# Kernel optimization log

Measured on AMD Instinct MI355X. Metric: run time of the kernel, lower is better.

## Reference

```python
import jax, jax.numpy as jnp
import numpy as np

EDGE_WIDTH = 128
NUM_HEADS = 8
DOT_DIM = EDGE_WIDTH // NUM_HEADS  # 16
B, N = 2, 256


def _layernorm(x, g, b, eps=1e-5):
    mu = jnp.mean(x, axis=-1, keepdims=True)
    var = jnp.var(x, axis=-1, keepdims=True)
    return (x - mu) * jax.lax.rsqrt(var + eps) * g + b


def setup_inputs() -> dict:
    key = jax.random.key(0)
    ks = jax.random.split(key, 8)
    W = EDGE_WIDTH
    H = NUM_HEADS
    s = lambda fan_in: 1.0 / np.sqrt(fan_in)
    return {
        "e": jax.random.normal(ks[0], (B, N, N, W), dtype=jnp.float32),
        "mask": jnp.zeros((B, N, N, 1), dtype=jnp.float32),
        "ln_g": jnp.ones((W,), dtype=jnp.float32),
        "ln_b": jnp.zeros((W,), dtype=jnp.float32),
        "W_V": jax.random.uniform(ks[1], (W, 2 * W), jnp.float32, -s(W), s(W)),
        "b_V": jnp.zeros((2 * W,), dtype=jnp.float32),
        "W_E": jax.random.uniform(ks[2], (W, 2 * H), jnp.float32, -s(W), s(W)),
        "b_E": jnp.zeros((2 * H,), dtype=jnp.float32),
        "W_O": jax.random.uniform(ks[3], (2 * W, W), jnp.float32, -s(2 * W), s(2 * W)),
        "b_O": jnp.zeros((W,), dtype=jnp.float32),
    }


def reference(e, mask, ln_g, ln_b, W_V, b_V, W_E, b_E, W_O, b_O):
    bsize, num_edges, _, embed_dim = e.shape
    H, D = NUM_HEADS, DOT_DIM

    e_ln = _layernorm(e, ln_g, ln_b)

    V = e_ln @ W_V + b_V                       # [B,N,N,2W]
    V_in, V_out = jnp.split(V, 2, axis=-1)     # each [B,N,N,W]
    V_in = V_in.reshape(bsize, num_edges, num_edges, D, H)
    V_out = V_out.reshape(bsize, num_edges, num_edges, D, H)

    E = e_ln @ W_E + b_E                       # [B,N,N,2H]
    E_in, E_out = jnp.split(E, 2, axis=-1)     # each [B,N,N,H]

    # NOTE: original module computes a scale factor but never applies it.
    A_in = jax.nn.softmax(E_in + mask, axis=2)            # softmax over k
    Va_in = jnp.einsum('bikh,bjkdh->bijdh', A_in, V_in)

    A_out = jax.nn.softmax(E_out + mask, axis=1)          # softmax over k
    Va_out = jnp.einsum('bkih,bkjdh->bijdh', A_out, V_out)

    Va = jnp.concatenate([Va_in, Va_out], axis=-1)        # [B,N,N,D,2H]
    Va = Va.reshape(bsize, num_edges, num_edges, embed_dim * 2)
    return Va @ W_O + b_O
```

## Files before the change

### kernel.cpp

```cpp
#include <hip/hip_runtime.h>
#include <hip/hip_bf16.h>
#include <stdint.h>


typedef short short8 __attribute__((ext_vector_type(8)));
typedef short short4v __attribute__((ext_vector_type(4)));
typedef float floatx4 __attribute__((ext_vector_type(4)));

#define AS1(p) ((const __attribute__((address_space(1))) void*)(p))
#define AS3(p) ((__attribute__((address_space(3))) void*)(p))

__device__ inline short f2bf(float v) {
    uint32_t u = __builtin_bit_cast(uint32_t, v);
    u += 0x7FFFu + ((u >> 16) & 1u);
    return (short)(u >> 16);
}

__global__ __launch_bounds__(128) void k0_prep(const float* __restrict__ WV,
                                               const float* __restrict__ WE,
                                               const float* __restrict__ WO,
                                               short* __restrict__ Wcat2,
                                               short* __restrict__ WOt2,
                                               const float* __restrict__ bV,
                                               const float* __restrict__ bE,
                                               float* __restrict__ bcat) {
    int bx = blockIdx.x, t = threadIdx.x;
    if (bx < 288) {
        int v = bx / 144, n = bx % 144, k = t;
        float val = 0.f;
        if (n < 128) val = WV[k * 256 + v * 128 + n];
        else if (n < 136) val = WE[k * 16 + v * 8 + (n - 128)];
        Wcat2[(v * 144 + n) * 128 + k] = f2bf(val);
    } else if (bx < 320) {
        int cc = bx - 288;
        for (int j = 0; j < 8; ++j) {
            int c = cc * 8 + j;
            WOt2[(cc * 128 + t) * 8 + j] =
                f2bf(WO[((c & 15) * 16 + (c >> 4)) * 128 + t]);
        }
    } else {
        for (int it = 0; it < 3; ++it) {
            int idx = it * 128 + t;
            if (idx < 288) {
                int v = idx / 144, n = idx % 144;
                float val = 0.f;
                if (n < 128) val = bV[v * 128 + n];
                else if (n < 136) val = bE[v * 8 + (n - 128)];
                bcat[idx] = val;
            }
        }
    }
}

__global__ __launch_bounds__(256, 2) void k1_ln_proj(
    const float* __restrict__ e, const float* __restrict__ ln_g,
    const float* __restrict__ ln_b, const float* __restrict__ mask,
    const short* __restrict__ Wcat2, const float* __restrict__ bcat,
    short* __restrict__ VinT, short* __restrict__ VoutT,
    short* __restrict__ Ain, short* __restrict__ AoutT) {
    __shared__ short At[256 * 128];
    __shared__ float maskb[256];
    __shared__ float redm[4][8];
    __shared__ float reds[4][8];

    const int tid = threadIdx.x;
    const int fix = blockIdx.x;
    const int b = blockIdx.y;
    const int v = blockIdx.z;
    const int estride = v ? 256 : 1;
    const size_t ebase = (size_t)b * 65536 + (size_t)fix * (v ? 1 : 256);
    const short* Wv = Wcat2 + v * 144 * 128;
    const float* bc = bcat + v * 144;
    short* Vdst = v ? VoutT : VinT;
    short* Adst = v ? AoutT : Ain;

    maskb[tid] = mask[(size_t)b * 65536 + (v ? (size_t)tid * 256 + fix
                                             : (size_t)fix * 256 + tid)];

    {
        const int rq = tid & 3;
        const int rowi = tid >> 2;
#pragma unroll
        for (int pass = 0; pass < 4; ++pass) {
            int row = pass * 64 + rowi;
            const float* ep = e + (ebase + (size_t)row * estride) * 128 + rq * 4;
            float4 val[8];
            float s = 0.f, s2 = 0.f;
#pragma unroll
            for (int i = 0; i < 8; ++i) {
                val[i] = *(const float4*)(ep + i * 16);
                s += val[i].x + val[i].y + val[i].z + val[i].w;
                s2 += val[i].x * val[i].x + val[i].y * val[i].y +
                      val[i].z * val[i].z + val[i].w * val[i].w;
            }
            s += __shfl_xor(s, 1); s2 += __shfl_xor(s2, 1);
            s += __shfl_xor(s, 2); s2 += __shfl_xor(s2, 2);
            float mean = s * 0.0078125f;
            float var = s2 * 0.0078125f - mean * mean;
            float rs = rsqrtf(var + 1e-5f);
#pragma unroll
            for (int i = 0; i < 8; ++i) {
                int col = i * 16 + rq * 4;
                float4 gg = *(const float4*)(ln_g + col);
                float4 bb = *(const float4*)(ln_b + col);
                short4v o;
                o[0] = f2bf((val[i].x - mean) * rs * gg.x + bb.x);
                o[1] = f2bf((val[i].y - mean) * rs * gg.y + bb.y);
                o[2] = f2bf((val[i].z - mean) * rs * gg.z + bb.z);
                o[3] = f2bf((val[i].w - mean) * rs * gg.w + bb.w);
                int g = col >> 3;
                int cp = g ^ (row & 15);
                int half = (col >> 2) & 1;
                *(short4v*)&At[row * 128 + cp * 8 + half * 4] = o;
            }
        }
    }
    __syncthreads();

    const int lane = tid & 63, w = tid >> 6;
    const int ln_ = lane & 15, quad = lane >> 4;
    float vE[16];

#pragma unroll
    for (int chunk = 0; chunk < 2; ++chunk) {
        floatx4 acc[4][4] = {};
#pragma unroll
        for (int kk = 0; kk < 4; ++kk) {
            int ckb = kk * 4 + quad;
            int cp = ckb ^ ln_;
            short8 aq[4];
#pragma unroll
            for (int mt = 0; mt < 4; ++mt) {
                int r = w * 64 + mt * 16 + ln_;
                aq[mt] = *(const short8*)&At[r * 128 + cp * 8];
            }
            short8 bq[4];
#pragma unroll
            for (int ntl = 0; ntl < 4; ++ntl) {
                int n = chunk * 64 + ntl * 16 + ln_;
                bq[ntl] = *(const short8*)(Wv + n * 128 + ckb * 8);
            }
#pragma unroll
            for (int mt = 0; mt < 4; ++mt)
#pragma unroll
                for (int ntl = 0; ntl < 4; ++ntl)
                    acc[mt][ntl] = __builtin_amdgcn_mfma_f32_16x16x32_bf16(
                        aq[mt], bq[ntl], acc[mt][ntl], 0, 0, 0);
        }
#pragma unroll
        for (int ntl = 0; ntl < 4; ++ntl) {
            int c = chunk * 64 + ntl * 16 + ln_;
            float bias = bc[c];
            int d = c >> 3, hh = c & 7;
            size_t rowbase = (((size_t)(b * 8 + hh) * 256 + fix) * 16 + d) * 256;
#pragma unroll
            for (int mt = 0; mt < 4; ++mt) {
                short4v o;
#pragma unroll
                for (int r = 0; r < 4; ++r) o[r] = f2bf(acc[mt][ntl][r] + bias);
                *(short4v*)(Vdst + rowbase + w * 64 + mt * 16 + quad * 4) = o;
            }
        }
    }

    {
        floatx4 accE[4] = {};
#pragma unroll
        for (int kk = 0; kk < 4; ++kk) {
            int ckb = kk * 4 + quad;
            int cp = ckb ^ ln_;
            short8 bq = *(const short8*)(Wv + (128 + ln_) * 128 + ckb * 8);
#pragma unroll
            for (int mt = 0; mt < 4; ++mt) {
                int r = w * 64 + mt * 16 + ln_;
                short8 aq = *(const short8*)&At[r * 128 + cp * 8];
                accE[mt] = __builtin_amdgcn_mfma_f32_16x16x32_bf16(
                    aq, bq, accE[mt], 0, 0, 0);
            }
        }
        float bias = bc[128 + ln_];
#pragma unroll
        for (int mt = 0; mt < 4; ++mt)
#pragma unroll
            for (int r = 0; r < 4; ++r) {
                int k = w * 64 + mt * 16 + quad * 4 + r;
                vE[mt * 4 + r] = accE[mt][r] + bias + maskb[k];
            }
    }

    {
        float m = vE[0];
#pragma unroll
        for (int i = 1; i < 16; ++i) m = fmaxf(m, vE[i]);
        m = fmaxf(m, __shfl_xor(m, 16));
        m = fmaxf(m, __shfl_xor(m, 32));
        if (quad == 0 && ln_ < 8) redm[w][ln_] = m;
        __syncthreads();
        int hs = ln_ & 7;
        float bmax = fmaxf(fmaxf(redm[0][hs], redm[1][hs]),
                           fmaxf(redm[2][hs], redm[3][hs]));
        float p[16], s = 0.f;
#pragma unroll
        for (int i = 0; i < 16; ++i) { p[i] = __expf(vE[i] - bmax); s += p[i]; }
        s += __shfl_xor(s, 16);
        s += __shfl_xor(s, 32);
        if (quad == 0 && ln_ < 8) reds[w][ln_] = s;
        __syncthreads();
        float inv = 1.f / (reds[0][hs] + reds[1][hs] + reds[2][hs] + reds[3][hs]);
        if (ln_ < 8) {
            size_t rowbase = (size_t)(b * 8 + ln_) * 65536 + (size_t)fix * 256;
#pragma unroll
            for (int mt = 0; mt < 4; ++mt) {
                short4v o;
#pragma unroll
                for (int r = 0; r < 4; ++r) o[r] = f2bf(p[mt * 4 + r] * inv);
                *(short4v*)(Adst + rowbase + w * 64 + mt * 16 + quad * 4) = o;
            }
        }
    }
}

__global__ __launch_bounds__(256, 3) void k3_einsum(const short* __restrict__ Ain,
                                                    const short* __restrict__ AoutT,
                                                    const short* __restrict__ VinT,
                                                    const short* __restrict__ VoutT,
                                                    short* __restrict__ VaP2) {
    __shared__ short AB[17408];
    const int tid = threadIdx.x, lane = tid & 63, w = tid >> 6;
    const int i0 = blockIdx.x * 128;
    const int jd0 = blockIdx.y * 128;
    const int z = blockIdx.z;
    const int b = z >> 4, part = (z >> 3) & 1, h = z & 7;

    const short* Abase = (part ? AoutT : Ain) + ((size_t)(b * 8 + h)) * 65536 + (size_t)i0 * 256;
    const short* Bbase = (part ? VoutT : VinT) + ((size_t)(b * 8 + h)) * 1048576 + (size_t)jd0 * 256;

    const int ln_ = lane & 15, quad = lane >> 4;
    const int m0 = (w >> 1) * 64, n0 = (w & 1) * 64;
    floatx4 acc[4][4] = {};

    for (int kt = 0; kt < 4; ++kt) {
        if (kt) __syncthreads();
        for (int it = 0; it < 8; ++it) {
            int cid = w * 512 + it * 64 + lane;
            int isB = cid >> 10;
            int lc = cid & 1023;
            int r = lc >> 3;
            int ck = (lc & 7) ^ (r & 7);
            const short* g = (isB ? Bbase : Abase) + r * 256 + kt * 64 + ck * 8;
            __builtin_amdgcn_global_load_lds(AS1(g), AS3(&AB[cid * 8]), 16, 0, 0);
        }
        __syncthreads();

#pragma unroll
        for (int kk = 0; kk < 2; ++kk) {
            int ckb = kk * 4 + quad;
            short8 aq[4], bq[4];
#pragma unroll
            for (int t = 0; t < 4; ++t) {
                int r = m0 + t * 16 + ln_;
                aq[t] = *(const short8*)&AB[(r * 8 + (ckb ^ (r & 7))) * 8];
            }
#pragma unroll
            for (int t = 0; t < 4; ++t) {
                int r = n0 + t * 16 + ln_;
                bq[t] = *(const short8*)&AB[(1024 + r * 8 + (ckb ^ (r & 7))) * 8];
            }
#pragma unroll
            for (int mt = 0; mt < 4; ++mt)
#pragma unroll
                for (int nt = 0; nt < 4; ++nt)
                    acc[mt][nt] = __builtin_amdgcn_mfma_f32_16x16x32_bf16(aq[mt], bq[nt], acc[mt][nt], 0, 0, 0);
        }
    }

    __syncthreads();
#pragma unroll
    for (int mt = 0; mt < 4; ++mt)
#pragma unroll
        for (int nt = 0; nt < 4; ++nt)
#pragma unroll
            for (int r = 0; r < 4; ++r) {
                int il = m0 + mt * 16 + quad * 4 + r;
                int jd = n0 + nt * 16 + ln_;
                AB[il * 136 + jd] = f2bf(acc[mt][nt][r]);
            }
    __syncthreads();

    const int ph = part * 8 + h;
    const int j0 = jd0 >> 4;
#pragma unroll
    for (int pp = 0; pp < 4; ++pp) {
        int pid = pp * 256 + tid;
        int il = pid >> 3, jl = pid & 7;
        size_t m = ((size_t)b * 256 + i0 + il) * 256 + j0 + jl;
        short8 v0 = *(const short8*)&AB[il * 136 + jl * 16];
        short8 v1 = *(const short8*)&AB[il * 136 + jl * 16 + 8];
        short* dst = VaP2 + ((size_t)ph * 131072 + m) * 16;
        *(short8*)dst = v0;
        *(short8*)(dst + 8) = v1;
    }
}

__global__ __launch_bounds__(256, 3) void k4_proj(const short* __restrict__ VaP2,
                                                  const short* __restrict__ WOt2,
                                                  const float* __restrict__ bO,
                                                  float* __restrict__ out) {
    __shared__ short A_s[16384];
    const int tid = threadIdx.x, lane = tid & 63, w = tid >> 6;
    const size_t m0g = (size_t)blockIdx.x * 128;
    const int ln_ = lane & 15, quad = lane >> 4;
    const int m0 = w * 32;
    floatx4 acc[2][8] = {};

    for (int kt = 0; kt < 2; ++kt) {
        if (kt) __syncthreads();
        for (int it = 0; it < 8; ++it) {
            int cid = w * 512 + it * 64 + lane;
            int p = cid >> 8, rm = cid & 255, half = rm >> 7, m = rm & 127;
            const short* g = VaP2 + ((size_t)(kt * 8 + p) * 131072 + m0g + m) * 16 + half * 8;
            __builtin_amdgcn_global_load_lds(AS1(g), AS3(&A_s[cid * 8]), 16, 0, 0);
        }
        __syncthreads();

#pragma unroll
        for (int kk = 0; kk < 4; ++kk) {
            int ckb = kk * 4 + quad;
            int p = ckb >> 1, hf = ckb & 1;
            short8 aq[2], bq[8];
#pragma unroll
            for (int mt = 0; mt < 2; ++mt) {
                int m = m0 + mt * 16 + ln_;
                aq[mt] = *(const short8*)&A_s[p * 2048 + hf * 1024 + m * 8];
            }
#pragma unroll
            for (int nt = 0; nt < 8; ++nt) {
                int wr = nt * 16 + ln_;
                bq[nt] = *(const short8*)(WOt2 + ((kt * 16 + ckb) * 128 + wr) * 8);
            }
#pragma unroll
            for (int mt = 0; mt < 2; ++mt)
#pragma unroll
                for (int nt = 0; nt < 8; ++nt)
                    acc[mt][nt] = __builtin_amdgcn_mfma_f32_16x16x32_bf16(aq[mt], bq[nt], acc[mt][nt], 0, 0, 0);
        }
    }

    float bo[8];
#pragma unroll
    for (int nt = 0; nt < 8; ++nt) bo[nt] = bO[nt * 16 + ln_];

#pragma unroll
    for (int mt = 0; mt < 2; ++mt)
#pragma unroll
        for (int r = 0; r < 4; ++r) {
            size_t mb = m0g + m0 + mt * 16 + quad * 4 + r;
#pragma unroll
            for (int nt = 0; nt < 8; ++nt)
                out[mb * 128 + nt * 16 + ln_] = acc[mt][nt][r] + bo[nt];
        }
}

extern "C" void kernel_launch(void* const* d_in, const int* in_sizes, int n_in,
                              void* d_out, int out_size, void* d_ws, size_t ws_size,
                              hipStream_t stream) {
    (void)in_sizes; (void)n_in; (void)out_size; (void)ws_size;
    const float* e    = (const float*)d_in[0];
    const float* mask = (const float*)d_in[1];
    const float* ln_g = (const float*)d_in[2];
    const float* ln_b = (const float*)d_in[3];
    const float* W_V  = (const float*)d_in[4];
    const float* b_V  = (const float*)d_in[5];
    const float* W_E  = (const float*)d_in[6];
    const float* b_E  = (const float*)d_in[7];
    const float* W_O  = (const float*)d_in[8];
    const float* b_O  = (const float*)d_in[9];
    float* out = (float*)d_out;

    char* ws = (char*)d_ws;
    short* VinT  = (short*)(ws + 0);
    short* VoutT = (short*)(ws + 33554432);
    short* Ain   = (short*)(ws + 67108864);
    short* AoutT = (short*)(ws + 69206016);
    short* VaP2  = (short*)(ws + 71303168);
    short* Wcat2 = (short*)(ws + 138412032);
    short* WOt2  = (short*)(ws + 138485760);
    float* bcat  = (float*)(ws + 138551296);

    k0_prep<<<321, 128, 0, stream>>>(W_V, W_E, W_O, Wcat2, WOt2, b_V, b_E, bcat);
    k1_ln_proj<<<dim3(256, 2, 2), 256, 0, stream>>>(e, ln_g, ln_b, mask, Wcat2,
                                                    bcat, VinT, VoutT, Ain, AoutT);
    k3_einsum<<<dim3(2, 32, 32), 256, 0, stream>>>(Ain, AoutT, VinT, VoutT, VaP2);
    k4_proj<<<1024, 256, 0, stream>>>(VaP2, WOt2, b_O, out);
}
```

Before: 225.3 us.

## Fold layernorm affine into weights and load A fragments directly into registers

The LayerNorm gain and bias are folded into the projection weights and biases in the prep kernel, so k1 only normalises. k1 now reads e straight into MFMA A-operand register fragments instead of staging a 64KB LDS tile. The LDS is reused to hold the swizzled weight matrix via global_load_lds, so B operands are read from LDS rather than global memory. Occupancy is raised to 3 blocks per CU, at the cost of more register pressure and uncoalesced per-row e loads.

New measurement: 269.0 us. +19.4%, slower.

```diff
diff --git a/kernel.cpp b/kernel.cpp
--- a/kernel.cpp
+++ b/kernel.cpp
@@ -19,6 +19,8 @@
 __global__ __launch_bounds__(128) void k0_prep(const float* __restrict__ WV,
                                                const float* __restrict__ WE,
                                                const float* __restrict__ WO,
+                                               const float* __restrict__ ln_g,
+                                               const float* __restrict__ ln_b,
                                                short* __restrict__ Wcat2,
                                                short* __restrict__ WOt2,
                                                const float* __restrict__ bV,
@@ -30,7 +32,7 @@
         float val = 0.f;
         if (n < 128) val = WV[k * 256 + v * 128 + n];
         else if (n < 136) val = WE[k * 16 + v * 8 + (n - 128)];
-        Wcat2[(v * 144 + n) * 128 + k] = f2bf(val);
+        Wcat2[(v * 144 + n) * 128 + k] = f2bf(val * ln_g[k]);
     } else if (bx < 320) {
         int cc = bx - 288;
         for (int j = 0; j < 8; ++j) {
@@ -43,22 +45,30 @@
             int idx = it * 128 + t;
             if (idx < 288) {
                 int v = idx / 144, n = idx % 144;
-                float val = 0.f;
-                if (n < 128) val = bV[v * 128 + n];
-                else if (n < 136) val = bE[v * 8 + (n - 128)];
-                bcat[idx] = val;
-            }
-        }
-    }
-}
-
-__global__ __launch_bounds__(256, 2) void k1_ln_proj(
+                float val = 0.f, dot = 0.f;
+                if (n < 128) {
+                    val = bV[v * 128 + n];
+                    for (int k = 0; k < 128; ++k)
+                        dot += ln_b[k] * WV[k * 256 + v * 128 + n];
+                } else if (n < 136) {
+                    val = bE[v * 8 + (n - 128)];
+                    for (int k = 0; k < 128; ++k)
+                        dot += ln_b[k] * WE[k * 16 + v * 8 + (n - 128)];
+                }
+                bcat[idx] = val + dot;
+            }
+        }
+    }
+}
+
+__global__ __launch_bounds__(256, 3) void k1_ln_proj(
     const float* __restrict__ e, const float* __restrict__ ln_g,
     const float* __restrict__ ln_b, const float* __restrict__ mask,
     const short* __restrict__ Wcat2, const float* __restrict__ bcat,
     short* __restrict__ VinT, short* __restrict__ VoutT,
     short* __restrict__ Ain, short* __restrict__ AoutT) {
-    __shared__ short At[256 * 128];
+    (void)ln_g; (void)ln_b;
+    __shared__ short Wlds[144 * 128];
     __shared__ float maskb[256];
     __shared__ float redm[4][8];
     __shared__ float reds[4][8];
@@ -74,51 +84,59 @@
     short* Vdst = v ? VoutT : VinT;
     short* Adst = v ? AoutT : Ain;
 
+    const int lane = tid & 63, w = tid >> 6;
+    const int ln_ = lane & 15, quad = lane >> 4;
+
+#pragma unroll
+    for (int it = 0; it < 9; ++it) {
+        int gid = it * 256 + tid;
+        int r = gid >> 4, p = gid & 15;
+        const short* src = Wv + (r * 16 + (p ^ (r & 15))) * 8;
+        __builtin_amdgcn_global_load_lds(AS1(src), AS3(&Wlds[gid * 8]), 16, 0, 0);
+    }
+
     maskb[tid] = mask[(size_t)b * 65536 + (v ? (size_t)tid * 256 + fix
                                              : (size_t)fix * 256 + tid)];
 
-    {
-        const int rq = tid & 3;
-        const int rowi = tid >> 2;
-#pragma unroll
-        for (int pass = 0; pass < 4; ++pass) {
-            int row = pass * 64 + rowi;
-            const float* ep = e + (ebase + (size_t)row * estride) * 128 + rq * 4;
-            float4 val[8];
-            float s = 0.f, s2 = 0.f;
-#pragma unroll
-            for (int i = 0; i < 8; ++i) {
-                val[i] = *(const float4*)(ep + i * 16);
-                s += val[i].x + val[i].y + val[i].z + val[i].w;
-                s2 += val[i].x * val[i].x + val[i].y * val[i].y +
-                      val[i].z * val[i].z + val[i].w * val[i].w;
-            }
-            s += __shfl_xor(s, 1); s2 += __shfl_xor(s2, 1);
-            s += __shfl_xor(s, 2); s2 += __shfl_xor(s2, 2);
-            float mean = s * 0.0078125f;
-            float var = s2 * 0.0078125f - mean * mean;
-            float rs = rsqrtf(var + 1e-5f);
-#pragma unroll
-            for (int i = 0; i < 8; ++i) {
-                int col = i * 16 + rq * 4;
-                float4 gg = *(const float4*)(ln_g + col);
-                float4 bb = *(const float4*)(ln_b + col);
-                short4v o;
-                o[0] = f2bf((val[i].x - mean) * rs * gg.x + bb.x);
-                o[1] = f2bf((val[i].y - mean) * rs * gg.y + bb.y);
-                o[2] = f2bf((val[i].z - mean) * rs * gg.z + bb.z);
-                o[3] = f2bf((val[i].w - mean) * rs * gg.w + bb.w);
-                int g = col >> 3;
-                int cp = g ^ (row & 15);
-                int half = (col >> 2) & 1;
-                *(short4v*)&At[row * 128 + cp * 8 + half * 4] = o;
-            }
+    short8 a_frag[4][4];
+#pragma unroll
+    for (int mt = 0; mt < 4; ++mt) {
+        int row = w * 64 + mt * 16 + ln_;
+        const float* ep = e + (ebase + (size_t)row * estride) * 128 + quad * 8;
+        float4 c0[4], c1[4];
+        float s = 0.f, s2 = 0.f;
+#pragma unroll
+        for (int kk = 0; kk < 4; ++kk) {
+            c0[kk] = *(const float4*)(ep + kk * 32);
+            c1[kk] = *(const float4*)(ep + kk * 32 + 4);
+            s += c0[kk].x + c0[kk].y + c0[kk].z + c0[kk].w +
+                 c1[kk].x + c1[kk].y + c1[kk].z + c1[kk].w;
+            s2 += c0[kk].x * c0[kk].x + c0[kk].y * c0[kk].y +
+                  c0[kk].z * c0[kk].z + c0[kk].w * c0[kk].w +
+                  c1[kk].x * c1[kk].x + c1[kk].y * c1[kk].y +
+                  c1[kk].z * c1[kk].z + c1[kk].w * c1[kk].w;
+        }
+        s += __shfl_xor(s, 16); s2 += __shfl_xor(s2, 16);
+        s += __shfl_xor(s, 32); s2 += __shfl_xor(s2, 32);
+        float mean = s * 0.0078125f;
+        float var = s2 * 0.0078125f - mean * mean;
+        float rs = rsqrtf(var + 1e-5f);
+#pragma unroll
+        for (int kk = 0; kk < 4; ++kk) {
+            short8 o;
+            o[0] = f2bf((c0[kk].x - mean) * rs);
+            o[1] = f2bf((c0[kk].y - mean) * rs);
+            o[2] = f2bf((c0[kk].z - mean) * rs);
+            o[3] = f2bf((c0[kk].w - mean) * rs);
+            o[4] = f2bf((c1[kk].x - mean) * rs);
+            o[5] = f2bf((c1[kk].y - mean) * rs);
+            o[6] = f2bf((c1[kk].z - mean) * rs);
+            o[7] = f2bf((c1[kk].w - mean) * rs);
+            a_frag[mt][kk] = o;
         }
     }
     __syncthreads();
 
-    const int lane = tid & 63, w = tid >> 6;
-    const int ln_ = lane & 15, quad = lane >> 4;
     float vE[16];
 
 #pragma unroll
@@ -127,25 +145,18 @@
 #pragma unroll
         for (int kk = 0; kk < 4; ++kk) {
             int ckb = kk * 4 + quad;
-            int cp = ckb ^ ln_;
-            short8 aq[4];
-#pragma unroll
-            for (int mt = 0; mt < 4; ++mt) {
-                int r = w * 64 + mt * 16 + ln_;
-                aq[mt] = *(const short8*)&At[r * 128 + cp * 8];
-            }
             short8 bq[4];
 #pragma unroll
             for (int ntl = 0; ntl < 4; ++ntl) {
                 int n = chunk * 64 + ntl * 16 + ln_;
-                bq[ntl] = *(const short8*)(Wv + n * 128 + ckb * 8);
+                bq[ntl] = *(const short8*)&Wlds[(n * 16 + (ckb ^ (n & 15))) * 8];
             }
 #pragma unroll
             for (int mt = 0; mt < 4; ++mt)
 #pragma unroll
                 for (int ntl = 0; ntl < 4; ++ntl)
                     acc[mt][ntl] = __builtin_amdgcn_mfma_f32_16x16x32_bf16(
-                        aq[mt], bq[ntl], acc[mt][ntl], 0, 0, 0);
+                        a_frag[mt][kk], bq[ntl], acc[mt][ntl], 0, 0, 0);
         }
 #pragma unroll
         for (int ntl = 0; ntl < 4; ++ntl) {
@@ -168,15 +179,12 @@
 #pragma unroll
         for (int kk = 0; kk < 4; ++kk) {
             int ckb = kk * 4 + quad;
-            int cp = ckb ^ ln_;
-            short8 bq = *(const short8*)(Wv + (128 + ln_) * 128 + ckb * 8);
-#pragma unroll
-            for (int mt = 0; mt < 4; ++mt) {
-                int r = w * 64 + mt * 16 + ln_;
-                short8 aq = *(const short8*)&At[r * 128 + cp * 8];
+            int n = 128 + ln_;
+            short8 bq = *(const short8*)&Wlds[(n * 16 + (ckb ^ (n & 15))) * 8];
+#pragma unroll
+            for (int mt = 0; mt < 4; ++mt)
                 accE[mt] = __builtin_amdgcn_mfma_f32_16x16x32_bf16(
-                    aq, bq, accE[mt], 0, 0, 0);
-            }
+                    a_frag[mt][kk], bq, accE[mt], 0, 0, 0);
         }
         float bias = bc[128 + ln_];
 #pragma unroll
@@ -387,7 +395,8 @@
     short* WOt2  = (short*)(ws + 138485760);
     float* bcat  = (float*)(ws + 138551296);
 
-    k0_prep<<<321, 128, 0, stream>>>(W_V, W_E, W_O, Wcat2, WOt2, b_V, b_E, bcat);
+    k0_prep<<<321, 128, 0, stream>>>(W_V, W_E, W_O, ln_g, ln_b, Wcat2, WOt2,
+                                     b_V, b_E, bcat);
     k1_ln_proj<<<dim3(256, 2, 2), 256, 0, stream>>>(e, ln_g, ln_b, mask, Wcat2,
                                                     bcat, VinT, VoutT, Ain, AoutT);
     k3_einsum<<<dim3(2, 32, 32), 256, 0, stream>>>(Ain, AoutT, VinT, VoutT, VaP2);
```
